# Performance work log

Hardware: AMD Instinct MI355X
Metric: run time of the kernel (lower is better)

Reference implementation:

```python
import jax, jax.numpy as jnp
import numpy as np

NQ, NK, H, DH = 1024, 512, 8, 64


def setup_inputs() -> dict:
    key = jax.random.key(0)
    ks = jax.random.split(key, 8)
    b, n, d, g = 4, 4096, 1024, 4
    di = H * DH  # 512
    s = lambda fan: 1.0 / np.sqrt(fan)
    return {
        "x": jax.random.normal(ks[0], (b, n, d), jnp.float32),
        "w_qr": jax.random.normal(ks[1], (g, d), jnp.float32) * s(d),
        "w_kvr": jax.random.normal(ks[2], (g, d), jnp.float32) * s(d),
        "w_q": jax.random.normal(ks[3], (g, di, d), jnp.float32) * s(d),
        "w_kv": jax.random.normal(ks[4], (g, 2 * di, d), jnp.float32) * s(d),
        "w_out": jax.random.normal(ks[5], (g, d, di), jnp.float32) * s(di),
        "null_kv": jax.random.normal(ks[6], (2, g, H, 1, DH), jnp.float32),
        "null_token": jax.random.normal(ks[7], (1, 1, d), jnp.float32),
    }


def reference(x, w_qr, w_kvr, w_q, w_kv, w_out, null_kv, null_token):
    b, n, d = x.shape
    g = w_qr.shape[0]
    bidx = jnp.arange(b)[:, None, None]
    # --- routing: per-expert token scores, top-k select (router reference) ---
    q_logits = jnp.einsum("bnd,gd->bgn", x, w_qr)
    q_top, q_idx = jax.lax.top_k(q_logits, NQ)            # [b,g,NQ]
    q_scores = jax.nn.sigmoid(q_top)[..., None]           # [b,g,NQ,1]
    queries = x[bidx, q_idx]                              # [b,g,NQ,d]
    kv_logits = jnp.einsum("bnd,gd->bgn", x, w_kvr)
    kv_top, kv_idx = jax.lax.top_k(kv_logits, NK)
    kv_scores = jax.nn.sigmoid(kv_top)[:, :, None, :, None]  # [b,g,1,NK,1]
    key_values = x[bidx, kv_idx]                          # [b,g,NK,d]
    # --- grouped attention (1x1 grouped convs == per-group matmuls) ---
    q = jnp.einsum("bgnd,ged->bgne", queries, w_q)
    kv = jnp.einsum("bgnd,ged->bgne", key_values, w_kv)
    k, v = jnp.split(kv, 2, axis=-1)
    heads = lambda t: t.reshape(b, g, -1, H, DH).transpose(0, 1, 3, 2, 4)  # b g h n dh
    q, k, v = heads(q), heads(k), heads(v)
    v = v * kv_scores                                     # values_scale
    nk = jnp.broadcast_to(null_kv[0][None], (b, g, H, 1, DH))
    nv = jnp.broadcast_to(null_kv[1][None], (b, g, H, 1, DH))
    k = jnp.concatenate([nk, k], axis=-2)
    v = jnp.concatenate([nv, v], axis=-2)
    attn = jax.nn.softmax(jnp.einsum("bghid,bghjd->bghij", q, k) * DH ** -0.5, axis=-1)
    o = jnp.einsum("bghij,bghjd->bghid", attn, v)
    o = o.transpose(0, 1, 3, 2, 4).reshape(b, g, NQ, H * DH)
    o = jnp.einsum("bgne,gde->bgnd", o, w_out)
    o = o * q_scores
    # --- scatter-add back with count normalization ---
    flat_idx = q_idx.reshape(b, g * NQ)
    flat_o = o.reshape(b, g * NQ, d)
    b2 = jnp.arange(b)[:, None]
    summed = jnp.zeros_like(x).at[b2, flat_idx].add(flat_o)
    counts = jnp.zeros((b, n), x.dtype).at[b2, flat_idx].add(1.0)[..., None]
    meaned = summed / jnp.clip(counts, 1e-5)
    return jnp.where(counts > 0, meaned, null_token)
```

## Files before the change

kernel.cpp:

```cpp
#include <hip/hip_runtime.h>
#include <math.h>

#define NB 4
#define SEQ 4096
#define DM 1024
#define NG 4
#define DI 512
#define NQS 1024
#define NKS 512
#define NHD 8
#define DHD 64
#define VTS 520

typedef unsigned int u32;
typedef unsigned short u16;
typedef __bf16 bf16x8 __attribute__((ext_vector_type(8)));
typedef float f32x4 __attribute__((ext_vector_type(4)));

__device__ __forceinline__ float bf2f(u16 u) { return __uint_as_float(((u32)u) << 16); }
__device__ __forceinline__ u16 f2bf(float f) {
  u32 u = __float_as_uint(f);
  u32 r = (u + 0x7FFFu + ((u >> 16) & 1u)) >> 16;
  return (u16)r;
}
__device__ __forceinline__ u16 f2bfh(float f) {
  union { __bf16 b; u16 u; } cv;
  cv.b = (__bf16)f;
  return cv.u;
}

__global__ __launch_bounds__(256) void router_kernel(
    const float* __restrict__ x, const float* __restrict__ wqr,
    const float* __restrict__ wkvr, float* __restrict__ qlog,
    float* __restrict__ kvlog, u16* __restrict__ xbf,
    const float* __restrict__ wq, const float* __restrict__ wkv,
    const float* __restrict__ wout, u16* __restrict__ wqbf,
    u16* __restrict__ wkvbf, u16* __restrict__ woutbf) {
  int tid = threadIdx.x;
#pragma unroll
  for (int j = 0; j < 2; j++) {
    int idx = blockIdx.x * 512 + j * 256 + tid;
    const float* src; u16* dst; int off;
    if (idx < 524288)        { src = wq;   dst = wqbf;   off = idx; }
    else if (idx < 1572864)  { src = wkv;  dst = wkvbf;  off = idx - 524288; }
    else                     { src = wout; dst = woutbf; off = idx - 1572864; }
    float4 v = ((const float4*)src)[off];
    ushort4 o;
    o.x = f2bf(v.x); o.y = f2bf(v.y); o.z = f2bf(v.z); o.w = f2bf(v.w);
    ((ushort4*)dst)[off] = o;
  }

  int widx = blockIdx.x * 4 + (tid >> 6);
  int lane = tid & 63;
  int b = widx >> 12, tok = widx & 4095;
  const float4* xr = (const float4*)(x + ((size_t)(b * SEQ + tok)) * DM);
  float4 xv[4];
#pragma unroll
  for (int i = 0; i < 4; i++) xv[i] = xr[i * 64 + lane];
  ushort4* xrow = (ushort4*)(xbf + ((size_t)(b * SEQ + tok)) * DM);
#pragma unroll
  for (int i = 0; i < 4; i++) {
    ushort4 o;
    o.x = f2bf(xv[i].x); o.y = f2bf(xv[i].y);
    o.z = f2bf(xv[i].z); o.w = f2bf(xv[i].w);
    xrow[i * 64 + lane] = o;
  }
  float accs[8];
#pragma unroll
  for (int r = 0; r < 8; r++) {
    const float4* wr =
        (const float4*)(r < 4 ? wqr + (r << 10) : wkvr + ((r - 4) << 10));
    float a = 0.f;
#pragma unroll
    for (int i = 0; i < 4; i++) {
      float4 w4 = wr[i * 64 + lane];
      a += xv[i].x * w4.x + xv[i].y * w4.y + xv[i].z * w4.z + xv[i].w * w4.w;
    }
    accs[r] = a;
  }
#pragma unroll
  for (int r = 0; r < 8; r++) {
    float a = accs[r];
#pragma unroll
    for (int off = 32; off >= 1; off >>= 1) a += __shfl_xor(a, off);
    if (lane == 0) {
      if (r < 4) qlog[((b << 2) | r) * SEQ + tok] = a;
      else kvlog[((b << 2) | (r - 4)) * SEQ + tok] = a;
    }
  }
}

__global__ __launch_bounds__(256) void topk_kernel(
    const float* __restrict__ qlog, const float* __restrict__ kvlog,
    int* __restrict__ qidx, float* __restrict__ qscore,
    int* __restrict__ kvidx, float* __restrict__ kvscore,
    int* __restrict__ qpos) {
  __shared__ u32 keys[4096];
  __shared__ int eqlist[2048];
  __shared__ int scnt[4];
  __shared__ int s_gt, s_eq;
  int which = blockIdx.x >> 4;
  int bg = blockIdx.x & 15;
  int K = (which == 0) ? NQS : NKS;
  const float* L = ((which == 0) ? qlog : kvlog) + bg * 4096;
  int* out_idx = ((which == 0) ? qidx : kvidx) + bg * K;
  float* out_score = ((which == 0) ? qscore : kvscore) + bg * K;
  int* qposb = qpos + bg * 4096;
  int tid = threadIdx.x;
  for (int e = tid; e < 4096; e += 256) {
    u32 u = __float_as_uint(L[e]);
    keys[e] = (u >> 31) ? ~u : (u | 0x80000000u);
  }
  if (which == 0)
    for (int e = tid; e < 4096; e += 256) qposb[e] = -1;
  if (tid == 0) { s_gt = 0; s_eq = 0; }
  __syncthreads();
  u32 prefix = 0;
  int remaining = K;
  for (int bit = 31; bit >= 0; --bit) {
    u32 want = prefix | (1u << bit);
    u32 mask = ~((1u << bit) - 1u);
    int c = 0;
    for (int e = tid; e < 4096; e += 256) c += ((keys[e] & mask) == want) ? 1 : 0;
#pragma unroll
    for (int off = 32; off >= 1; off >>= 1) c += __shfl_xor(c, off);
    if ((tid & 63) == 0) scnt[tid >> 6] = c;
    __syncthreads();
    int total = scnt[0] + scnt[1] + scnt[2] + scnt[3];
    if (total >= remaining) prefix = want;
    else remaining -= total;
    __syncthreads();
  }
  u32 T = prefix;
  for (int e = tid; e < 4096; e += 256) {
    u32 k = keys[e];
    if (k > T) {
      int pos = atomicAdd(&s_gt, 1);
      out_idx[pos] = e;
      u32 uo = (k >> 31) ? (k & 0x7FFFFFFFu) : ~k;
      float v = __uint_as_float(uo);
      out_score[pos] = 1.0f / (1.0f + __expf(-v));
      if (which == 0) qposb[e] = pos;
    } else if (k == T) {
      int p = atomicAdd(&s_eq, 1);
      if (p < 2048) eqlist[p] = e;
    }
  }
  __syncthreads();
  int gt = s_gt;
  int eq = min(s_eq, 2048);
  int need = K - gt;
  for (int i = tid; i < eq; i += 256) {
    int my = eqlist[i];
    int rank = 0;
    for (int j = 0; j < eq; j++) rank += (eqlist[j] < my) ? 1 : 0;
    if (rank < need) {
      int pos = gt + rank;
      out_idx[pos] = my;
      u32 k2 = keys[my];
      u32 uo = (k2 >> 31) ? (k2 & 0x7FFFFFFFu) : ~k2;
      float v = __uint_as_float(uo);
      out_score[pos] = 1.0f / (1.0f + __expf(-v));
      if (which == 0) qposb[my] = pos;
    }
  }
}

struct Ptr4 { const u16* p[4]; };

__device__ __forceinline__ void mfma_core(Ptr4 A, Ptr4 B, u16* Asm, u16* Bsm,
                                          int ktiles, int tid, f32x4 (&acc)[4][4]) {
  int w = tid >> 6, lane = tid & 63;
  int col = lane & 15, quad = lane >> 4;
  int wr = w >> 1, wc = w & 1;
  for (int kt = 0; kt < ktiles; kt++) {
#pragma unroll
    for (int r = 0; r < 4; r++) {
      char* ldsA = (char*)Asm + (r * 256 + w * 64) * 16;
      __builtin_amdgcn_global_load_lds(
          (const __attribute__((address_space(1))) void*)(A.p[r] + kt * 64),
          (__attribute__((address_space(3))) void*)ldsA, 16, 0, 0);
    }
#pragma unroll
    for (int r = 0; r < 4; r++) {
      char* ldsB = (char*)Bsm + (r * 256 + w * 64) * 16;
      __builtin_amdgcn_global_load_lds(
          (const __attribute__((address_space(1))) void*)(B.p[r] + kt * 64),
          (__attribute__((address_space(3))) void*)ldsB, 16, 0, 0);
    }
    __syncthreads();
#pragma unroll
    for (int k04 = 0; k04 < 8; k04 += 4) {
      bf16x8 af[4], bfr[4];
#pragma unroll
      for (int t = 0; t < 4; t++) {
        int rowa = wr * 64 + t * 16 + col;
        int sp = (quad + k04) ^ (col & 7);
        af[t] = *(const bf16x8*)((const char*)Asm + (rowa * 8 + sp) * 16);
        int rowb = wc * 64 + t * 16 + col;
        bfr[t] = *(const bf16x8*)((const char*)Bsm + (rowb * 8 + sp) * 16);
      }
#pragma unroll
      for (int t = 0; t < 4; t++)
#pragma unroll
        for (int u = 0; u < 4; u++)
          acc[t][u] = __builtin_amdgcn_mfma_f32_16x16x32_bf16(af[t], bfr[u], acc[t][u], 0, 0, 0);
    }
    __syncthreads();
  }
}

__global__ __launch_bounds__(256) void gemm_qkvproj(
    const u16* __restrict__ xbf, const int* __restrict__ qidx,
    const int* __restrict__ kvidx, const u16* __restrict__ wqbf,
    const u16* __restrict__ wkvbf, const float* __restrict__ kvscore,
    u16* __restrict__ qbuf, u16* __restrict__ kbuf, u16* __restrict__ vtbuf) {
  __shared__ __align__(16) u16 Asm[8192], Bsm[8192];
  __shared__ int ridx[128];
  int tid = threadIdx.x;
  int id = blockIdx.x;
  bool is_q = (id & 1) == 0;
  int sid = id >> 1;
  int bg = sid >> 5, r5 = sid & 31;
  int b = bg >> 2, g = bg & 3;
  int w = tid >> 6, lane = tid & 63;
  int col = lane & 15, quad = lane >> 4;
  int wr = w >> 1, wc = w & 1;

  if (is_q) {
    int col0 = (r5 & 3) * 128, row0 = (r5 >> 2) * 128;
    if (tid < 128) ridx[tid] = qidx[bg * NQS + row0 + tid];
    __syncthreads();
    Ptr4 A, B;
#pragma unroll
    for (int r = 0; r < 4; r++) {
      int G = r * 256 + tid;
      int row = G >> 3;
      int seg = (G & 7) ^ (row & 7);
      A.p[r] = xbf + ((size_t)b * SEQ + ridx[row]) * DM + seg * 8;
      B.p[r] = wqbf + ((size_t)g * DI + col0 + row) * DM + seg * 8;
    }
    f32x4 acc[4][4] = {};
    mfma_core(A, B, Asm, Bsm, DM / 64, tid, acc);
#pragma unroll
    for (int t = 0; t < 4; t++)
#pragma unroll
      for (int u = 0; u < 4; u++)
#pragma unroll
        for (int r = 0; r < 4; r++) {
          int rowg = row0 + wr * 64 + t * 16 + quad * 4 + r;
          int colg = col0 + wc * 64 + u * 16 + col;
          qbuf[((size_t)bg * NQS + rowg) * DI + colg] = f2bf(acc[t][u][r] * 0.125f);
        }
  } else {
    int col0 = (r5 & 7) * 128, row0 = (r5 >> 3) * 128;
    if (tid < 128) ridx[tid] = kvidx[bg * NKS + row0 + tid];
    __syncthreads();
    Ptr4 A, B;
#pragma unroll
    for (int r = 0; r < 4; r++) {
      int G = r * 256 + tid;
      int row = G >> 3;
      int seg = (G & 7) ^ (row & 7);
      A.p[r] = xbf + ((size_t)b * SEQ + ridx[row]) * DM + seg * 8;
      B.p[r] = wkvbf + ((size_t)g * (2 * DI) + col0 + row) * DM + seg * 8;
    }
    f32x4 acc[4][4] = {};
    mfma_core(A, B, Asm, Bsm, DM / 64, tid, acc);
    if (col0 < DI) {
#pragma unroll
      for (int t = 0; t < 4; t++)
#pragma unroll
        for (int u = 0; u < 4; u++)
#pragma unroll
          for (int r = 0; r < 4; r++) {
            int rowg = row0 + wr * 64 + t * 16 + quad * 4 + r;
            int colg = col0 + wc * 64 + u * 16 + col;
            kbuf[((size_t)bg * NKS + rowg) * DI + colg] = f2bf(acc[t][u][r]);
          }
    } else {
#pragma unroll
      for (int t = 0; t < 4; t++) {
        int base = row0 + wr * 64 + t * 16 + quad * 4;
        float sc0 = kvscore[bg * NKS + base + 0];
        float sc1 = kvscore[bg * NKS + base + 1];
        float sc2 = kvscore[bg * NKS + base + 2];
        float sc3 = kvscore[bg * NKS + base + 3];
#pragma unroll
        for (int u = 0; u < 4; u++) {
          int vc = col0 - DI + wc * 64 + u * 16 + col;
          int h = vc >> 6, d = vc & 63;
          u32 lo = (u32)f2bf(acc[t][u][0] * sc0) | ((u32)f2bf(acc[t][u][1] * sc1) << 16);
          u32 hi = (u32)f2bf(acc[t][u][2] * sc2) | ((u32)f2bf(acc[t][u][3] * sc3) << 16);
          *(uint2*)&vtbuf[(((size_t)bg * NHD + h) * DHD + d) * VTS + base] =
              make_uint2(lo, hi);
        }
      }
    }
  }
}

__global__ __launch_bounds__(256) void gemm_outproj(
    const u16* __restrict__ obuf, const u16* __restrict__ woutbf,
    const float* __restrict__ qscore, float* __restrict__ oproj_lo,
    float* __restrict__ oproj_hi) {
  int bg = blockIdx.z, g = bg & 3;
  int row0 = blockIdx.y * 128, col0 = blockIdx.x * 128;
  __shared__ __align__(16) u16 Asm[8192], Bsm[8192];
  int tid = threadIdx.x;
  Ptr4 A, B;
#pragma unroll
  for (int r = 0; r < 4; r++) {
    int G = r * 256 + tid;
    int row = G >> 3;
    int seg = (G & 7) ^ (row & 7);
    A.p[r] = obuf + ((size_t)bg * NQS + row0 + row) * DI + seg * 8;
    B.p[r] = woutbf + ((size_t)g * DM + col0 + row) * DI + seg * 8;
  }
  f32x4 acc[4][4] = {};
  mfma_core(A, B, Asm, Bsm, DI / 64, tid, acc);
  int w = tid >> 6, lane = tid & 63;
  int col = lane & 15, quad = lane >> 4;
  int wr = w >> 1, wc = w & 1;
  float* obase = (bg < 8 ? oproj_lo : oproj_hi) + (size_t)(bg & 7) * NQS * DM;
#pragma unroll
  for (int t = 0; t < 4; t++)
#pragma unroll
    for (int r = 0; r < 4; r++) {
      int rowg = row0 + wr * 64 + t * 16 + quad * 4 + r;
      float sc = qscore[bg * NQS + rowg];
      float* orow = obase + (size_t)rowg * DM;
#pragma unroll
      for (int u = 0; u < 4; u++) {
        int colg = col0 + wc * 64 + u * 16 + col;
        orow[colg] = acc[t][u][r] * sc;
      }
    }
}

__global__ __launch_bounds__(256) void finalize_gather(
    const float* __restrict__ oproj_lo, const float* __restrict__ oproj_hi,
    const int* __restrict__ qpos, const float* __restrict__ null_token,
    float* __restrict__ dout) {
  int blk = blockIdx.x;
  int b = blk >> 12;
  int tok = blk & 4095;
  int tid = threadIdx.x;
  const float* obase = (b < 2) ? oproj_lo : oproj_hi;
  int zoff = (b & 1) * 4;
  float4 acc = {0.f, 0.f, 0.f, 0.f};
  int cnt = 0;
#pragma unroll
  for (int g = 0; g < 4; g++) {
    int pos = qpos[(((b << 2) | g)) * 4096 + tok];
    if (pos >= 0) {
      const float4* row =
          (const float4*)(obase + ((size_t)(zoff + g) * NQS + pos) * DM);
      float4 v = row[tid];
      acc.x += v.x; acc.y += v.y; acc.z += v.z; acc.w += v.w;
      cnt++;
    }
  }
  float4* dst = (float4*)(dout + ((size_t)b * SEQ + tok) * DM) + tid;
  if (cnt > 0) {
    float inv = 1.0f / cnt;
    acc.x *= inv; acc.y *= inv; acc.z *= inv; acc.w *= inv;
    *dst = acc;
  } else {
    *dst = ((const float4*)null_token)[tid];
  }
}

__global__ __launch_bounds__(256, 4) void attn_mfma(
    const u16* __restrict__ qbuf, const u16* __restrict__ kbuf,
    const u16* __restrict__ vtbuf, const float* __restrict__ null_kv,
    u16* __restrict__ obuf) {
  int qt = blockIdx.x;
  int h = blockIdx.y;
  int bg = blockIdx.z;
  int g = bg & 3;
  int tid = threadIdx.x;
  int w = tid >> 6, lane = tid & 63;
  int col = lane & 15, quad = lane >> 4;

  __shared__ __align__(16) u16 Ks[64][72];
  __shared__ __align__(16) u16 Vts[64][72];
  __shared__ __align__(16) u16 Ps[4][32][72];

  int q0 = qt * 128 + w * 32;
  const u16* qp0 = qbuf + ((size_t)bg * NQS + q0 + col) * DI + h * DHD + quad * 8;
  bf16x8 qa[2][2];
  qa[0][0] = *(const bf16x8*)qp0;
  qa[0][1] = *(const bf16x8*)(qp0 + 32);
  qa[1][0] = *(const bf16x8*)(qp0 + 16 * DI);
  qa[1][1] = *(const bf16x8*)(qp0 + 16 * DI + 32);

  const float* kn = null_kv + ((size_t)(0 * NG + g) * NHD + h) * DHD;
  const float* vn = null_kv + ((size_t)(1 * NG + g) * NHD + h) * DHD;
  float m_run[2], l_lane[2];
  f32x4 oacc[2][4];
#pragma unroll
  for (int s = 0; s < 2; s++) {
    float sn = 0.f;
#pragma unroll
    for (int i = 0; i < 8; i++) {
      sn += (float)qa[s][0][i] * kn[quad * 8 + i];
      sn += (float)qa[s][1][i] * kn[32 + quad * 8 + i];
    }
    sn += __shfl_xor(sn, 16);
    sn += __shfl_xor(sn, 32);
    m_run[s] = sn;
    l_lane[s] = (quad == 0) ? 1.f : 0.f;
  }
#pragma unroll
  for (int t = 0; t < 4; t++) {
    float v = vn[t * 16 + col];
    f32x4 tmp = {v, v, v, v};
    oacc[0][t] = tmp;
    oacc[1][t] = tmp;
  }

  int sr = tid >> 2, ss = tid & 3;
  const u16* kptr = kbuf + ((size_t)bg * NKS + sr) * DI + h * DHD + ss * 16;
  const u16* vptr = vtbuf + (((size_t)bg * NHD + h) * DHD + sr) * VTS + ss * 16;
  uint4* kdst = (uint4*)&Ks[sr][ss * 16];
  uint4* vdst = (uint4*)&Vts[sr][ss * 16];
  uint4 ck0, ck1, cv0, cv1;
  { const uint4* p = (const uint4*)kptr; ck0 = p[0]; ck1 = p[1]; }
  { const uint4* p = (const uint4*)vptr; cv0 = p[0]; cv1 = p[1]; }

  for (int c = 0; c < 8; ++c) {
    kdst[0] = ck0; kdst[1] = ck1;
    vdst[0] = cv0; vdst[1] = cv1;
    if (c < 7) {
      const uint4* p = (const uint4*)(kptr + (size_t)(c + 1) * 64 * DI);
      ck0 = p[0]; ck1 = p[1];
      const uint4* q4 = (const uint4*)(vptr + (c + 1) * 64);
      cv0 = q4[0]; cv1 = q4[1];
    }
    __syncthreads();

    f32x4 sv[2][4];
    __builtin_amdgcn_s_setprio(1);
#pragma unroll
    for (int t = 0; t < 4; t++) {
      bf16x8 kb0 = *(const bf16x8*)&Ks[t * 16 + col][quad * 8];
      bf16x8 kb1 = *(const bf16x8*)&Ks[t * 16 + col][quad * 8 + 32];
      f32x4 z = {0.f, 0.f, 0.f, 0.f};
      f32x4 s0 = __builtin_amdgcn_mfma_f32_16x16x32_bf16(kb0, qa[0][0], z, 0, 0, 0);
      sv[0][t] = __builtin_amdgcn_mfma_f32_16x16x32_bf16(kb1, qa[0][1], s0, 0, 0, 0);
      f32x4 s1 = __builtin_amdgcn_mfma_f32_16x16x32_bf16(kb0, qa[1][0], z, 0, 0, 0);
      sv[1][t] = __builtin_amdgcn_mfma_f32_16x16x32_bf16(kb1, qa[1][1], s1, 0, 0, 0);
    }
    __builtin_amdgcn_s_setprio(0);

#pragma unroll
    for (int s = 0; s < 2; s++) {
      float pm = sv[s][0][0];
#pragma unroll
      for (int t = 0; t < 4; t++)
#pragma unroll
        for (int r = 0; r < 4; r++) pm = fmaxf(pm, sv[s][t][r]);
      pm = fmaxf(pm, __shfl_xor(pm, 16));
      pm = fmaxf(pm, __shfl_xor(pm, 32));
      if (!__all(pm <= m_run[s] + 8.0f)) {
        float mnew = fmaxf(m_run[s], pm);
        float alpha = __expf(m_run[s] - mnew);
        m_run[s] = mnew;
        l_lane[s] *= alpha;
#pragma unroll
        for (int r = 0; r < 4; r++) {
          float a_o = __shfl(alpha, quad * 4 + r);
#pragma unroll
          for (int t = 0; t < 4; t++) oacc[s][t][r] *= a_o;
        }
      }
      float rs = 0.f;
#pragma unroll
      for (int t = 0; t < 4; t++) {
        float p0 = __expf(sv[s][t][0] - m_run[s]);
        float p1 = __expf(sv[s][t][1] - m_run[s]);
        float p2 = __expf(sv[s][t][2] - m_run[s]);
        float p3 = __expf(sv[s][t][3] - m_run[s]);
        rs += (p0 + p1) + (p2 + p3);
        u32 lo = (u32)f2bfh(p0) | ((u32)f2bfh(p1) << 16);
        u32 hi = (u32)f2bfh(p2) | ((u32)f2bfh(p3) << 16);
        *(uint2*)&Ps[w][s * 16 + col][t * 16 + quad * 4] = make_uint2(lo, hi);
      }
      l_lane[s] += rs;
    }

    __builtin_amdgcn_s_setprio(1);
#pragma unroll
    for (int s2 = 0; s2 < 2; s2++) {
      bf16x8 pa0 = *(const bf16x8*)&Ps[w][col][s2 * 32 + quad * 8];
      bf16x8 pa1 = *(const bf16x8*)&Ps[w][16 + col][s2 * 32 + quad * 8];
#pragma unroll
      for (int t = 0; t < 4; t++) {
        bf16x8 vb = *(const bf16x8*)&Vts[t * 16 + col][s2 * 32 + quad * 8];
        oacc[0][t] = __builtin_amdgcn_mfma_f32_16x16x32_bf16(pa0, vb, oacc[0][t], 0, 0, 0);
        oacc[1][t] = __builtin_amdgcn_mfma_f32_16x16x32_bf16(pa1, vb, oacc[1][t], 0, 0, 0);
      }
    }
    __builtin_amdgcn_s_setprio(0);
    __syncthreads();
  }

#pragma unroll
  for (int s = 0; s < 2; s++) {
    float l = l_lane[s];
    l += __shfl_xor(l, 16);
    l += __shfl_xor(l, 32);
    float inv = 1.0f / l;
#pragma unroll
    for (int r = 0; r < 4; r++) {
      float ir = __shfl(inv, quad * 4 + r);
#pragma unroll
      for (int t = 0; t < 4; t++) {
        obuf[((size_t)bg * NQS + q0 + s * 16 + quad * 4 + r) * DI + h * DHD +
             t * 16 + col] = f2bfh(oacc[s][t][r] * ir);
      }
    }
  }
}

extern "C" void kernel_launch(void* const* d_in, const int* in_sizes, int n_in,
                              void* d_out, int out_size, void* d_ws, size_t ws_size,
                              hipStream_t stream) {
  const float* x = (const float*)d_in[0];
  const float* wqr = (const float*)d_in[1];
  const float* wkvr = (const float*)d_in[2];
  const float* wq = (const float*)d_in[3];
  const float* wkv = (const float*)d_in[4];
  const float* wout = (const float*)d_in[5];
  const float* nullkv = (const float*)d_in[6];
  const float* nulltok = (const float*)d_in[7];
  float* out = (float*)d_out;
  char* ws = (char*)d_ws;
  float* qlog = (float*)(ws + 0);
  float* kvlog = (float*)(ws + 262144);
  int* qidx = (int*)(ws + 524288);
  int* kvidx = (int*)(ws + 589824);
  float* qscore = (float*)(ws + 622592);
  float* kvscore = (float*)(ws + 688128);
  u16* qbuf = (u16*)(ws + 786432);
  u16* kbuf = (u16*)(ws + 17563648);
  u16* vtbuf = (u16*)(ws + 25952256);
  u16* obuf = (u16*)(ws + 34476032);
  u16* xbf = (u16*)(ws + 51253248);
  u16* wqbf = (u16*)(ws + 84807680);
  u16* wkvbf = (u16*)(ws + 89001984);
  u16* woutbf = (u16*)(ws + 97390592);
  int* qpos = (int*)(ws + 0);
  float* oproj_lo = (float*)(ws + 786432);
  float* oproj_hi = (float*)(ws + 51253248);

  router_kernel<<<4096, 256, 0, stream>>>(x, wqr, wkvr, qlog, kvlog, xbf, wq,
                                          wkv, wout, wqbf, wkvbf, woutbf);
  topk_kernel<<<32, 256, 0, stream>>>(qlog, kvlog, qidx, qscore, kvidx, kvscore,
                                      qpos);
  gemm_qkvproj<<<1024, 256, 0, stream>>>(xbf, qidx, kvidx, wqbf, wkvbf, kvscore,
                                         qbuf, kbuf, vtbuf);
  attn_mfma<<<dim3(8, 8, 16), 256, 0, stream>>>(qbuf, kbuf, vtbuf, nullkv, obuf);
  gemm_outproj<<<dim3(8, 8, 16), 256, 0, stream>>>(obuf, woutbf, qscore,
                                                   oproj_lo, oproj_hi);
  finalize_gather<<<16384, 256, 0, stream>>>(oproj_lo, oproj_hi, qpos, nulltok,
                                             out);
}
```

Measured before the change: 333.4 us.

## Move weight bf16 conversion into topk launch and process two tokens per router warp

The fp32-to-bf16 weight conversion moves out of the router kernel into 2048 extra blocks of the topk launch. Those blocks can fill the GPU while the 32 top-k blocks run their serial radix select. The router now has each wavefront handle two tokens, so each routing-weight load is reused twice. The s_setprio hints around the MFMA sections in attention are also removed. The topk kernel gets heavier, but its mostly idle CUs now do useful conversion work.

```diff
diff --git a/kernel.cpp b/kernel.cpp
--- a/kernel.cpp
+++ b/kernel.cpp
@@ -32,60 +32,60 @@
 __global__ __launch_bounds__(256) void router_kernel(
     const float* __restrict__ x, const float* __restrict__ wqr,
     const float* __restrict__ wkvr, float* __restrict__ qlog,
-    float* __restrict__ kvlog, u16* __restrict__ xbf,
-    const float* __restrict__ wq, const float* __restrict__ wkv,
-    const float* __restrict__ wout, u16* __restrict__ wqbf,
-    u16* __restrict__ wkvbf, u16* __restrict__ woutbf) {
+    float* __restrict__ kvlog, u16* __restrict__ xbf) {
   int tid = threadIdx.x;
-#pragma unroll
-  for (int j = 0; j < 2; j++) {
-    int idx = blockIdx.x * 512 + j * 256 + tid;
-    const float* src; u16* dst; int off;
-    if (idx < 524288)        { src = wq;   dst = wqbf;   off = idx; }
-    else if (idx < 1572864)  { src = wkv;  dst = wkvbf;  off = idx - 524288; }
-    else                     { src = wout; dst = woutbf; off = idx - 1572864; }
-    float4 v = ((const float4*)src)[off];
-    ushort4 o;
-    o.x = f2bf(v.x); o.y = f2bf(v.y); o.z = f2bf(v.z); o.w = f2bf(v.w);
-    ((ushort4*)dst)[off] = o;
-  }
-
-  int widx = blockIdx.x * 4 + (tid >> 6);
+  int base = blockIdx.x * 8 + (tid >> 6) * 2;
   int lane = tid & 63;
-  int b = widx >> 12, tok = widx & 4095;
-  const float4* xr = (const float4*)(x + ((size_t)(b * SEQ + tok)) * DM);
-  float4 xv[4];
-#pragma unroll
-  for (int i = 0; i < 4; i++) xv[i] = xr[i * 64 + lane];
-  ushort4* xrow = (ushort4*)(xbf + ((size_t)(b * SEQ + tok)) * DM);
+  int b = base >> 12, tok = base & 4095;
+  const float4* xr0 = (const float4*)(x + ((size_t)(b * SEQ + tok)) * DM);
+  const float4* xr1 = xr0 + 256;
+  float4 xv0[4], xv1[4];
 #pragma unroll
   for (int i = 0; i < 4; i++) {
-    ushort4 o;
-    o.x = f2bf(xv[i].x); o.y = f2bf(xv[i].y);
-    o.z = f2bf(xv[i].z); o.w = f2bf(xv[i].w);
-    xrow[i * 64 + lane] = o;
-  }
-  float accs[8];
+    xv0[i] = xr0[i * 64 + lane];
+    xv1[i] = xr1[i * 64 + lane];
+  }
+  ushort4* xrow0 = (ushort4*)(xbf + ((size_t)(b * SEQ + tok)) * DM);
+  ushort4* xrow1 = xrow0 + 256;
+#pragma unroll
+  for (int i = 0; i < 4; i++) {
+    ushort4 o0, o1;
+    o0.x = f2bf(xv0[i].x); o0.y = f2bf(xv0[i].y);
+    o0.z = f2bf(xv0[i].z); o0.w = f2bf(xv0[i].w);
+    o1.x = f2bf(xv1[i].x); o1.y = f2bf(xv1[i].y);
+    o1.z = f2bf(xv1[i].z); o1.w = f2bf(xv1[i].w);
+    xrow0[i * 64 + lane] = o0;
+    xrow1[i * 64 + lane] = o1;
+  }
+  float a0[8], a1[8];
 #pragma unroll
   for (int r = 0; r < 8; r++) {
     const float4* wr =
         (const float4*)(r < 4 ? wqr + (r << 10) : wkvr + ((r - 4) << 10));
-    float a = 0.f;
+    float s0 = 0.f, s1 = 0.f;
 #pragma unroll
     for (int i = 0; i < 4; i++) {
       float4 w4 = wr[i * 64 + lane];
-      a += xv[i].x * w4.x + xv[i].y * w4.y + xv[i].z * w4.z + xv[i].w * w4.w;
-    }
-    accs[r] = a;
+      s0 += xv0[i].x * w4.x + xv0[i].y * w4.y + xv0[i].z * w4.z + xv0[i].w * w4.w;
+      s1 += xv1[i].x * w4.x + xv1[i].y * w4.y + xv1[i].z * w4.z + xv1[i].w * w4.w;
+    }
+    a0[r] = s0; a1[r] = s1;
   }
 #pragma unroll
   for (int r = 0; r < 8; r++) {
-    float a = accs[r];
-#pragma unroll
-    for (int off = 32; off >= 1; off >>= 1) a += __shfl_xor(a, off);
+#pragma unroll
+    for (int off = 32; off >= 1; off >>= 1) {
+      a0[r] += __shfl_xor(a0[r], off);
+      a1[r] += __shfl_xor(a1[r], off);
+    }
     if (lane == 0) {
-      if (r < 4) qlog[((b << 2) | r) * SEQ + tok] = a;
-      else kvlog[((b << 2) | (r - 4)) * SEQ + tok] = a;
+      if (r < 4) {
+        qlog[((b << 2) | r) * SEQ + tok] = a0[r];
+        qlog[((b << 2) | r) * SEQ + tok + 1] = a1[r];
+      } else {
+        kvlog[((b << 2) | (r - 4)) * SEQ + tok] = a0[r];
+        kvlog[((b << 2) | (r - 4)) * SEQ + tok + 1] = a1[r];
+      }
     }
   }
 }
@@ -94,7 +94,26 @@
     const float* __restrict__ qlog, const float* __restrict__ kvlog,
     int* __restrict__ qidx, float* __restrict__ qscore,
     int* __restrict__ kvidx, float* __restrict__ kvscore,
-    int* __restrict__ qpos) {
+    int* __restrict__ qpos, const float* __restrict__ wq,
+    const float* __restrict__ wkv, const float* __restrict__ wout,
+    u16* __restrict__ wqbf, u16* __restrict__ wkvbf, u16* __restrict__ woutbf) {
+  int tid = threadIdx.x;
+  if (blockIdx.x >= 32) {
+    int cid = blockIdx.x - 32;
+#pragma unroll
+    for (int j = 0; j < 4; j++) {
+      int idx = cid * 1024 + j * 256 + tid;
+      const float* src; u16* dst; int off;
+      if (idx < 524288)        { src = wq;   dst = wqbf;   off = idx; }
+      else if (idx < 1572864)  { src = wkv;  dst = wkvbf;  off = idx - 524288; }
+      else                     { src = wout; dst = woutbf; off = idx - 1572864; }
+      float4 v = ((const float4*)src)[off];
+      ushort4 o;
+      o.x = f2bf(v.x); o.y = f2bf(v.y); o.z = f2bf(v.z); o.w = f2bf(v.w);
+      ((ushort4*)dst)[off] = o;
+    }
+    return;
+  }
   __shared__ u32 keys[4096];
   __shared__ int eqlist[2048];
   __shared__ int scnt[4];
@@ -106,7 +125,6 @@
   int* out_idx = ((which == 0) ? qidx : kvidx) + bg * K;
   float* out_score = ((which == 0) ? qscore : kvscore) + bg * K;
   int* qposb = qpos + bg * 4096;
-  int tid = threadIdx.x;
   for (int e = tid; e < 4096; e += 256) {
     u32 u = __float_as_uint(L[e]);
     keys[e] = (u >> 31) ? ~u : (u | 0x80000000u);
@@ -441,7 +459,6 @@
     __syncthreads();
 
     f32x4 sv[2][4];
-    __builtin_amdgcn_s_setprio(1);
 #pragma unroll
     for (int t = 0; t < 4; t++) {
       bf16x8 kb0 = *(const bf16x8*)&Ks[t * 16 + col][quad * 8];
@@ -452,7 +469,6 @@
       f32x4 s1 = __builtin_amdgcn_mfma_f32_16x16x32_bf16(kb0, qa[1][0], z, 0, 0, 0);
       sv[1][t] = __builtin_amdgcn_mfma_f32_16x16x32_bf16(kb1, qa[1][1], s1, 0, 0, 0);
     }
-    __builtin_amdgcn_s_setprio(0);
 
 #pragma unroll
     for (int s = 0; s < 2; s++) {
@@ -490,7 +506,6 @@
       l_lane[s] += rs;
     }
 
-    __builtin_amdgcn_s_setprio(1);
 #pragma unroll
     for (int s2 = 0; s2 < 2; s2++) {
       bf16x8 pa0 = *(const bf16x8*)&Ps[w][col][s2 * 32 + quad * 8];
@@ -502,7 +517,6 @@
         oacc[1][t] = __builtin_amdgcn_mfma_f32_16x16x32_bf16(pa1, vb, oacc[1][t], 0, 0, 0);
       }
     }
-    __builtin_amdgcn_s_setprio(0);
     __syncthreads();
   }
 
@@ -555,10 +569,10 @@
   float* oproj_lo = (float*)(ws + 786432);
   float* oproj_hi = (float*)(ws + 51253248);
 
-  router_kernel<<<4096, 256, 0, stream>>>(x, wqr, wkvr, qlog, kvlog, xbf, wq,
-                                          wkv, wout, wqbf, wkvbf, woutbf);
-  topk_kernel<<<32, 256, 0, stream>>>(qlog, kvlog, qidx, qscore, kvidx, kvscore,
-                                      qpos);
+  router_kernel<<<2048, 256, 0, stream>>>(x, wqr, wkvr, qlog, kvlog, xbf);
+  topk_kernel<<<2080, 256, 0, stream>>>(qlog, kvlog, qidx, qscore, kvidx,
+                                        kvscore, qpos, wq, wkv, wout, wqbf,
+                                        wkvbf, woutbf);
   gemm_qkvproj<<<1024, 256, 0, stream>>>(xbf, qidx, kvidx, wqbf, wkvbf, kvscore,
                                          qbuf, kbuf, vtbuf);
   attn_mfma<<<dim3(8, 8, 16), 256, 0, stream>>>(qbuf, kbuf, vtbuf, nullkv, obuf);
```

New measurement: 316.7 us. -5.0%, faster.
